# Kernel optimization log

Hardware: AMD Instinct MI355X
Metric: run time of the kernel (lower is better)

## Reference

```python
import jax, jax.numpy as jnp
import numpy as np

D_MODEL = 32
NHEAD = 4
NUM_LAYERS = 4
WINDOW = 256
D_FF = 2 * D_MODEL
INPUT_DIM = 58
MAX_DEPTH = 12
HEAD_OUT = 25


def _layernorm(x, g, b, eps=1e-5):
    m = jnp.mean(x, axis=-1, keepdims=True)
    v = jnp.mean((x - m) ** 2, axis=-1, keepdims=True)
    return (x - m) / jnp.sqrt(v + eps) * g + b


def _layer(h, ipw, ipb, opw, opb, g1, b1, w1, bb1, w2, bb2, g2, b2):
    # Post-norm transformer layer (subclass overrides parent's norm_first path).
    Wn, S, D = h.shape
    dh = D // NHEAD
    qkv = h @ ipw.T + ipb                      # [Wn, S, 3D]
    q, k, v = jnp.split(qkv, 3, axis=-1)
    q = q.reshape(Wn, S, NHEAD, dh).transpose(0, 2, 1, 3)  # [Wn,H,S,dh]
    k = k.reshape(Wn, S, NHEAD, dh).transpose(0, 2, 1, 3)
    v = v.reshape(Wn, S, NHEAD, dh).transpose(0, 2, 1, 3)
    scores = jnp.einsum('whqd,whkd->whqk', q, k) / jnp.sqrt(jnp.asarray(dh, h.dtype))
    a = jax.nn.softmax(scores, axis=-1)        # eager attn weights (need_weights=True path)
    o = jnp.einsum('whqk,whkd->whqd', a, v).transpose(0, 2, 1, 3).reshape(Wn, S, D)
    o = o @ opw.T + opb
    h = _layernorm(h + o, g1, b1)
    ff = jax.nn.gelu(h @ w1.T + bb1, approximate=False) @ w2.T + bb2
    return _layernorm(h + ff, g2, b2)


def setup_inputs() -> dict:
    key = jax.random.key(0)
    ks = jax.random.split(key, 24)
    B, N = 2, 65536
    x = jax.random.uniform(ks[0], (B, N, INPUT_DIM), dtype=jnp.float32)
    layers = jax.random.randint(ks[1], (B, N), 0, MAX_DEPTH)

    def w(k, shape, s=0.05):
        return jax.random.normal(k, shape, jnp.float32) * s

    L = NUM_LAYERS
    return dict(
        x=x,
        layers=layers,
        feature_proj_w=w(ks[2], (D_MODEL, INPUT_DIM)),
        feature_proj_b=w(ks[3], (D_MODEL,)),
        layer_embed=w(ks[4], (MAX_DEPTH, D_MODEL)),
        fourier_B=jax.random.normal(ks[5], (3, D_MODEL // 2), jnp.float32) * 1024.0,
        in_proj_w=w(ks[6], (L, 3 * D_MODEL, D_MODEL)),
        in_proj_b=w(ks[7], (L, 3 * D_MODEL)),
        out_proj_w=w(ks[8], (L, D_MODEL, D_MODEL)),
        out_proj_b=w(ks[9], (L, D_MODEL)),
        ln1_g=jnp.ones((L, D_MODEL), jnp.float32),
        ln1_b=jnp.zeros((L, D_MODEL), jnp.float32),
        lin1_w=w(ks[10], (L, D_FF, D_MODEL)),
        lin1_b=w(ks[11], (L, D_FF)),
        lin2_w=w(ks[12], (L, D_MODEL, D_FF)),
        lin2_b=w(ks[13], (L, D_MODEL)),
        ln2_g=jnp.ones((L, D_MODEL), jnp.float32),
        ln2_b=jnp.zeros((L, D_MODEL), jnp.float32),
        norm_out_g=jnp.ones((D_MODEL,), jnp.float32),
        norm_out_b=jnp.zeros((D_MODEL,), jnp.float32),
        head_w=w(ks[14], (HEAD_OUT, D_MODEL)),
        head_b=w(ks[15], (HEAD_OUT,)),
    )


def reference(x, layers, feature_proj_w, feature_proj_b, layer_embed, fourier_B,
              in_proj_w, in_proj_b, out_proj_w, out_proj_b,
              ln1_g, ln1_b, lin1_w, lin1_b, lin2_w, lin2_b, ln2_g, ln2_b,
              norm_out_g, norm_out_b, head_w, head_b):
    B, N, _ = x.shape
    pos = x[:, :, :3]
    proj = (2.0 * jnp.pi) * (pos @ fourier_B)                  # [B,N,D/2]
    pe = jnp.concatenate([jnp.sin(proj), jnp.cos(proj)], axis=-1)
    h = x @ feature_proj_w.T + feature_proj_b + layer_embed[layers] + pe
    # N chosen divisible by WINDOW, so pad_len == 0 (original pads otherwise)
    nw = N // WINDOW
    h = h.reshape(B * nw, WINDOW, D_MODEL)
    for i in range(NUM_LAYERS):
        h = _layer(h, in_proj_w[i], in_proj_b[i], out_proj_w[i], out_proj_b[i],
                   ln1_g[i], ln1_b[i], lin1_w[i], lin1_b[i], lin2_w[i], lin2_b[i],
                   ln2_g[i], ln2_b[i])
    h = h.reshape(B, N, D_MODEL)
    return _layernorm(h, norm_out_g, norm_out_b) @ head_w.T + head_b
```

## Files before the change

### kernel.cpp

```cpp
#include <hip/hip_runtime.h>

constexpr int S    = 256;
constexpr int D    = 32;
constexpr int NH   = 4;
constexpr int DH   = 8;
constexpr int DFF  = 64;
constexpr int NL   = 4;
constexpr int IND  = 58;
constexpr int HOUT = 25;
constexpr int TPB  = 256;

typedef float  f2 __attribute__((ext_vector_type(2)));
typedef float  f4 __attribute__((ext_vector_type(4)));
typedef __fp16 h2 __attribute__((ext_vector_type(2)));
typedef __fp16 h4 __attribute__((ext_vector_type(4)));

__device__ __forceinline__ f4 MFMA16(h4 a, h4 b, f4 c) {
  return __builtin_amdgcn_mfma_f32_16x16x16f16(a, b, c, 0, 0, 0);
}

constexpr int HOFF  = 0;
constexpr int QKOFF = 16384;
constexpr int VOFF  = 49152;

__device__ __forceinline__ unsigned pk2(float a, float b) {
  h2 h = __builtin_amdgcn_cvt_pkrtz(a, b);
  return __builtin_bit_cast(unsigned, h);
}

__device__ __forceinline__ float exp2fast(float x) {
#if __has_builtin(__builtin_amdgcn_exp2f)
  return __builtin_amdgcn_exp2f(x);
#else
  return exp2f(x);
#endif
}

__device__ __forceinline__ void wave_fence() {
  __builtin_amdgcn_wave_barrier();
  __builtin_amdgcn_sched_barrier(0);
}

template<int NF2>
__device__ __forceinline__ float dotp(const float* __restrict__ w,
                                      const float* __restrict__ v) {
  const f2* W = (const f2*)w;
  const f2* V = (const f2*)v;
  f2 a0 = {0.f, 0.f}, a1 = {0.f, 0.f};
#pragma unroll
  for (int i = 0; i < NF2; i += 2) a0 += V[i] * W[i];
#pragma unroll
  for (int i = 1; i < NF2; i += 2) a1 += V[i] * W[i];
  f2 s = a0 + a1;
  return s.x + s.y;
}

__device__ __forceinline__ float gelu(float x) {
  float u = 2.3022082f * fmaf(0.044715f * x * x, x, x);
  return x * __builtin_amdgcn_rcpf(1.0f + exp2fast(-u));
}

__device__ __forceinline__ void lnorm(float* h, const float* __restrict__ g,
                                      const float* __restrict__ b) {
  f2* hv = (f2*)h;
  f2 s0 = hv[0], s1 = hv[1];
#pragma unroll
  for (int i = 2; i < 16; i += 2) { s0 += hv[i]; s1 += hv[i + 1]; }
  f2 s = s0 + s1;
  const float m = (s.x + s.y) * (1.0f / D);
  const f2 m2 = {m, m};
  f2 v0 = {0.f, 0.f}, v1 = {0.f, 0.f};
#pragma unroll
  for (int i = 0; i < 16; i += 2) {
    f2 c0 = hv[i] - m2;     v0 += c0 * c0;
    f2 c1 = hv[i + 1] - m2; v1 += c1 * c1;
  }
  f2 vs = v0 + v1;
  const float inv = __builtin_amdgcn_rsqf((vs.x + vs.y) * (1.0f / D) + 1e-5f);
  const f2 inv2 = {inv, inv};
  const f2 mi2 = {-m * inv, -m * inv};
  const f2* g2 = (const f2*)g;
  const f2* b2 = (const f2*)b;
#pragma unroll
  for (int i = 0; i < 16; ++i) {
    f2 t = hv[i] * inv2 + mi2;
    hv[i] = t * g2[i] + b2[i];
  }
}

__device__ __forceinline__ void embed_token(
    const float* __restrict__ xrow, int lay,
    const float* __restrict__ fpw, const float* __restrict__ fpb,
    const float* __restrict__ lemb, const float* __restrict__ fB,
    float* __restrict__ h) {
  float xr[IND];
  const f2* xv = (const f2*)xrow;
#pragma unroll
  for (int i = 0; i < 29; ++i) { f2 t = xv[i]; xr[2 * i] = t.x; xr[2 * i + 1] = t.y; }
  const float* le = lemb + lay * D;
  float pe[D];
#pragma unroll
  for (int k = 0; k < 16; ++k) {
    float t = xr[0] * fB[k] + xr[1] * fB[16 + k] + xr[2] * fB[32 + k];
#if __has_builtin(__builtin_amdgcn_sinf) && __has_builtin(__builtin_amdgcn_cosf) && __has_builtin(__builtin_amdgcn_fractf)
    float u = __builtin_amdgcn_fractf(t);
    pe[k]      = __builtin_amdgcn_sinf(u);
    pe[16 + k] = __builtin_amdgcn_cosf(u);
#else
    float sv, cv;
    sincosf(6.2831853071795864f * (t - floorf(t)), &sv, &cv);
    pe[k] = sv; pe[16 + k] = cv;
#endif
  }
#pragma unroll
  for (int d = 0; d < D; ++d)
    h[d] = dotp<29>(fpw + d * IND, xr) + fpb[d] + le[d] + pe[d];
}

__device__ __forceinline__ h4 bfrag(const float* __restrict__ W, int row,
                                    int K, int kh, int quad) {
  f4 w = *(const f4*)(W + row * K + kh * 16 + quad * 4);
  uint2 p{pk2(w.x, w.y), pk2(w.z, w.w)};
  return __builtin_bit_cast(h4, p);
}
__device__ __forceinline__ h4 afrag32(const unsigned char* sm, int base,
                                      int tok, int kh, int quad) {
  return *(const h4*)(sm + base + tok * 64 + (((kh * 4 + quad) ^ (tok & 7)) * 8));
}

__device__ __forceinline__ void store_h16(unsigned char* sm, int tok,
                                          const float* __restrict__ h) {
#pragma unroll
  for (int c = 0; c < 8; ++c) {
    uint2 p{pk2(h[4 * c], h[4 * c + 1]), pk2(h[4 * c + 2], h[4 * c + 3])};
    *(uint2*)(sm + HOFF + tok * 64 + ((c ^ (tok & 7)) * 8)) = p;
  }
}
__device__ __forceinline__ void add_row32(const unsigned char* sm, int base,
                                          int tok, float* __restrict__ h) {
  f2* hv = (f2*)h;
#pragma unroll
  for (int c = 0; c < 8; ++c) {
    h4 q = *(const h4*)(sm + base + tok * 64 + ((c ^ (tok & 7)) * 8));
    f2 lo = {(float)q[0], (float)q[1]};
    f2 hi = {(float)q[2], (float)q[3]};
    hv[2 * c] += lo;
    hv[2 * c + 1] += hi;
  }
}

__global__ void __launch_bounds__(TPB, 2)
spai_fused(const float* __restrict__ x,    const int*   __restrict__ layers,
           const float* __restrict__ fpw,  const float* __restrict__ fpb,
           const float* __restrict__ lemb, const float* __restrict__ fB,
           const float* __restrict__ ipw,  const float* __restrict__ ipb,
           const float* __restrict__ opw,  const float* __restrict__ opb,
           const float* __restrict__ ln1g, const float* __restrict__ ln1b,
           const float* __restrict__ w1,   const float* __restrict__ b1,
           const float* __restrict__ w2,   const float* __restrict__ b2,
           const float* __restrict__ ln2g, const float* __restrict__ ln2b,
           const float* __restrict__ nog,  const float* __restrict__ nob,
           const float* __restrict__ hw,   const float* __restrict__ hb,
           float* __restrict__ out) {
  __shared__ __align__(16) unsigned char sm[65536];
  const int tid  = threadIdx.x;
  const int lane = tid & 63;
  const int wave = tid >> 6;
  const int n16  = lane & 15;
  const int quad = lane >> 4;
  const int qs   = quad & 1;
  const size_t blk_tok = (size_t)blockIdx.x * S;

  float h[D];
  embed_token(x + (blk_tok + tid) * IND, layers[blk_tok + tid],
              fpw, fpb, lemb, fB, h);
  store_h16(sm, tid, h);

  for (int l = 0; l < NL; ++l) {
    __syncthreads();

    const float* Wi = ipw + l * (3 * D) * D;
    const float* Bi = ipb + l * (3 * D);

    {
      h4 Bf[12]; f4 bqk[4]; float bv[2];
#pragma unroll
      for (int nt = 0; nt < 6; ++nt) {
        const float sc = (nt < 2) ? 0.51006973f : 1.0f;
#pragma unroll
        for (int kh = 0; kh < 2; ++kh) {
          f4 wv = *(const f4*)(Wi + (nt * 16 + n16) * D + kh * 16 + quad * 4) * sc;
          uint2 wp{pk2(wv.x, wv.y), pk2(wv.z, wv.w)};
          Bf[nt * 2 + kh] = __builtin_bit_cast(h4, wp);
        }
        if (nt < 4)
          bqk[nt] = *(const f4*)(Bi + nt * 16 + quad * 4) * sc;
        else
          bv[nt - 4] = Bi[nt * 16 + n16];
      }
      h4 Ah[8];
#pragma unroll
      for (int it = 0; it < 4; ++it) {
        const int tok = (wave * 4 + it) * 16 + n16;
        Ah[it * 2]     = afrag32(sm, HOFF, tok, 0, quad);
        Ah[it * 2 + 1] = afrag32(sm, HOFF, tok, 1, quad);
      }
      const int kswz = n16 & 7;
#pragma unroll
      for (int it = 0; it < 4; ++it) {
        const int tok = (wave * 4 + it) * 16 + n16;
#pragma unroll
        for (int nt = 0; nt < 4; ++nt) {
          f4 C = bqk[nt];
          C = MFMA16(Bf[nt * 2], Ah[it * 2], C);
          C = MFMA16(Bf[nt * 2 + 1], Ah[it * 2 + 1], C);
          uint2 p{pk2(C[0], C[1]), pk2(C[2], C[3])};
          *(uint2*)(sm + QKOFF + tok * 128 +
                    (((nt * 2 + (quad >> 1)) ^ kswz) * 16) + (quad & 1) * 8) = p;
        }
#pragma unroll
        for (int nt = 4; nt < 6; ++nt) {
          const float bb = bv[nt - 4];
          f4 C = {bb, bb, bb, bb};
          C = MFMA16(Ah[it * 2], Bf[nt * 2], C);
          C = MFMA16(Ah[it * 2 + 1], Bf[nt * 2 + 1], C);
          uint2 p{pk2(C[0], C[1]), pk2(C[2], C[3])};
          const int vf = (nt - 4) * 16 + n16;
          const int tc = (wave * 4 + it) * 4 + quad;
          *(uint2*)(sm + VOFF + vf * 512 + ((tc ^ ((vf & 7) << 1)) * 8)) = p;
        }
      }
    }
    __syncthreads();

    {
      const int hh  = wave;
      const int m   = n16;
      const int msw = m & 7;
      h4 Kf[16], Vf[16];
      const int kbase = QKOFF + (((4 + hh) ^ msw) * 16) + qs * 8;
#pragma unroll
      for (int jt = 0; jt < 16; ++jt) {
        uint2 a = *(const uint2*)(sm + kbase + (jt * 16 + m) * 128);
        if (quad >= 2) { a.x = 0u; a.y = 0u; }
        Kf[jt] = __builtin_bit_cast(h4, a);
      }
      const unsigned fill = (m == 8) ? 0x3C003C00u : 0u;
      const int vbase = VOFF + (hh * 8 + msw) * 512;
      const int vkey  = msw << 1;
#pragma unroll
      for (int jt = 0; jt < 16; ++jt) {
        uint2 a = *(const uint2*)(sm + vbase + (((jt * 4 + quad) ^ vkey) * 8));
        if (m >= 8) { a.x = fill; a.y = fill; }
        Vf[jt] = __builtin_bit_cast(h4, a);
      }
      const int qoff = QKOFF + ((hh ^ msw) * 16) + qs * 8;
      const int ooff = HOFF + (((hh * 2 + quad) ^ msw) * 8);

#pragma unroll 2
      for (int it = 0; it < 16; ++it) {
        const int ti = it * 16 + m;
        h4 Qf = *(const h4*)(sm + qoff + ti * 128);
        f4 Of0 = {0.f, 0.f, 0.f, 0.f}, Of1 = {0.f, 0.f, 0.f, 0.f};
        const f4 Z = {0.f, 0.f, 0.f, 0.f};
#pragma unroll
        for (int jt = 0; jt < 16; ++jt) {
          f4 T = MFMA16(Kf[jt], Qf, Z);
          uint2 pu{pk2(exp2fast(T[0]), exp2fast(T[1])),
                   pk2(exp2fast(T[2]), exp2fast(T[3]))};
          h4 P = __builtin_bit_cast(h4, pu);
          if (jt & 1) Of1 = MFMA16(Vf[jt], P, Of1);
          else        Of0 = MFMA16(Vf[jt], P, Of0);
        }
        f4 Of = Of0 + Of1;
        float rinv = __builtin_amdgcn_rcpf(Of[0]);
        rinv = __builtin_bit_cast(
            float, __builtin_amdgcn_ds_bpermute(
                       (32 + m) << 2, __builtin_bit_cast(int, rinv)));
        if (quad < 2) {
          f4 o = Of * rinv;
          uint2 p{pk2(o[0], o[1]), pk2(o[2], o[3])};
          *(uint2*)(sm + ooff + ti * 64) = p;
        }
      }
    }
    __syncthreads();

    {
      const float* Wo = opw + l * D * D;
      const float* Bo = opb + l * D;
      h4 Bf[4]; f4 bo[2];
#pragma unroll
      for (int nt = 0; nt < 2; ++nt) {
        bo[nt] = *(const f4*)(Bo + nt * 16 + quad * 4);
#pragma unroll
        for (int kh = 0; kh < 2; ++kh)
          Bf[nt * 2 + kh] = bfrag(Wo, nt * 16 + n16, 32, kh, quad);
      }
      const int kswz = n16 & 7;
#pragma unroll
      for (int ii = 0; ii < 4; ++ii) {
        const int tok = (wave * 4 + ii) * 16 + n16;
        h4 A0 = afrag32(sm, HOFF, tok, 0, quad);
        h4 A1 = afrag32(sm, HOFF, tok, 1, quad);
#pragma unroll
        for (int nt = 0; nt < 2; ++nt) {
          f4 C = bo[nt];
          C = MFMA16(Bf[nt * 2], A0, C);
          C = MFMA16(Bf[nt * 2 + 1], A1, C);
          uint2 p{pk2(C[0], C[1]), pk2(C[2], C[3])};
          *(uint2*)(sm + VOFF + tok * 64 + (((nt * 4 + quad) ^ kswz) * 8)) = p;
        }
      }
    }
    wave_fence();

    add_row32(sm, VOFF, tid, h);
    lnorm(h, ln1g + l * D, ln1b + l * D);
    store_h16(sm, tid, h);
    wave_fence();

    {
      const float* Wa = w1 + l * DFF * D;
      const float* Ba = b1 + l * DFF;
      h4 Bf[8]; f4 ba[4];
#pragma unroll
      for (int ft = 0; ft < 4; ++ft) {
        ba[ft] = *(const f4*)(Ba + ft * 16 + quad * 4);
#pragma unroll
        for (int kh = 0; kh < 2; ++kh)
          Bf[ft * 2 + kh] = bfrag(Wa, ft * 16 + n16, 32, kh, quad);
      }
      const int tswz = n16;
#pragma unroll
      for (int tt = 0; tt < 4; ++tt) {
        const int tok = (wave * 4 + tt) * 16 + n16;
        h4 A0 = afrag32(sm, HOFF, tok, 0, quad);
        h4 A1 = afrag32(sm, HOFF, tok, 1, quad);
#pragma unroll
        for (int ft = 0; ft < 4; ++ft) {
          f4 C = ba[ft];
          C = MFMA16(Bf[ft * 2], A0, C);
          C = MFMA16(Bf[ft * 2 + 1], A1, C);
          uint2 p{pk2(gelu(C[0]), gelu(C[1])), pk2(gelu(C[2]), gelu(C[3]))};
          *(uint2*)(sm + QKOFF + tok * 128 + (((ft * 4 + quad) ^ tswz) * 8)) = p;
        }
      }
    }
    wave_fence();

    {
      const float* Wb = w2 + l * D * DFF;
      const float* Bb = b2 + l * D;
      h4 Bf[8]; f4 bb[2];
#pragma unroll
      for (int nt = 0; nt < 2; ++nt) {
        bb[nt] = *(const f4*)(Bb + nt * 16 + quad * 4);
#pragma unroll
        for (int kh = 0; kh < 4; ++kh)
          Bf[nt * 4 + kh] = bfrag(Wb, nt * 16 + n16, 64, kh, quad);
      }
      const int tswz = n16; const int kswz = n16 & 7;
#pragma unroll
      for (int ii = 0; ii < 4; ++ii) {
        const int tok = (wave * 4 + ii) * 16 + n16;
        h4 A[4];
#pragma unroll
        for (int kh = 0; kh < 4; ++kh)
          A[kh] = *(const h4*)(sm + QKOFF + tok * 128 +
                               (((kh * 4 + quad) ^ tswz) * 8));
#pragma unroll
        for (int nt = 0; nt < 2; ++nt) {
          f4 C = bb[nt];
#pragma unroll
          for (int kh = 0; kh < 4; ++kh) C = MFMA16(Bf[nt * 4 + kh], A[kh], C);
          uint2 p{pk2(C[0], C[1]), pk2(C[2], C[3])};
          *(uint2*)(sm + VOFF + tok * 64 + (((nt * 4 + quad) ^ kswz) * 8)) = p;
        }
      }
    }
    wave_fence();

    add_row32(sm, VOFF, tid, h);
    lnorm(h, ln2g + l * D, ln2b + l * D);
    if (l < NL - 1) store_h16(sm, tid, h);
  }

  __syncthreads();
  lnorm(h, nog, nob);
  float* hs = (float*)sm;
#pragma unroll
  for (int o = 0; o < HOUT; ++o)
    hs[tid * HOUT + o] = dotp<16>(hw + o * D, h) + hb[o];
  __syncthreads();
  f2* og = (f2*)(out + blk_tok * HOUT);
  const f2* os2 = (const f2*)hs;
  for (int i = tid; i < S * HOUT / 2; i += TPB) og[i] = os2[i];
}

extern "C" void kernel_launch(void* const* d_in, const int* in_sizes, int n_in,
                              void* d_out, int out_size, void* d_ws, size_t ws_size,
                              hipStream_t stream) {
  const float* x    = (const float*)d_in[0];
  const int*   lays = (const int*)  d_in[1];
  const float* fpw  = (const float*)d_in[2];
  const float* fpb  = (const float*)d_in[3];
  const float* lemb = (const float*)d_in[4];
  const float* fB   = (const float*)d_in[5];
  const float* ipw  = (const float*)d_in[6];
  const float* ipb  = (const float*)d_in[7];
  const float* opw  = (const float*)d_in[8];
  const float* opb  = (const float*)d_in[9];
  const float* ln1g = (const float*)d_in[10];
  const float* ln1b = (const float*)d_in[11];
  const float* w1   = (const float*)d_in[12];
  const float* b1   = (const float*)d_in[13];
  const float* w2   = (const float*)d_in[14];
  const float* b2   = (const float*)d_in[15];
  const float* ln2g = (const float*)d_in[16];
  const float* ln2b = (const float*)d_in[17];
  const float* nog  = (const float*)d_in[18];
  const float* nob  = (const float*)d_in[19];
  const float* hw   = (const float*)d_in[20];
  const float* hb   = (const float*)d_in[21];
  float* out = (float*)d_out;

  const int nwin = in_sizes[0] / (S * IND);
  spai_fused<<<nwin, TPB, 0, stream>>>(x, lays, fpw, fpb, lemb, fB, ipw, ipb,
                                       opw, opb, ln1g, ln1b, w1, b1, w2, b2,
                                       ln2g, ln2b, nog, nob, hw, hb, out);
}
```

Baseline: 240.5 us.

## Split each token across two threads and fuse FFN GEMMs in registers

Doubles the block to 512 threads so each token's 32-wide hidden state is held by two threads of 16 features each. LayerNorm and the output head combine the two halves with xor-shuffles, and the embedding computes only the half's sine or cosine via a quarter-phase shift. Attention and the projection GEMMs are re-partitioned over 8 waves. Separately, the two FFN matmuls are fused so the GELU outputs stay in registers as MFMA operands instead of round-tripping through shared memory. This trades per-thread register pressure and serial per-token work for more waves per block, at the cost of extra shuffles and duplicated weight-fragment loads per wave.

```diff
diff --git a/kernel.cpp b/kernel.cpp
--- a/kernel.cpp
+++ b/kernel.cpp
@@ -8,7 +8,7 @@
 constexpr int NL   = 4;
 constexpr int IND  = 58;
 constexpr int HOUT = 25;
-constexpr int TPB  = 256;
+constexpr int TPB  = 512;
 
 typedef float  f2 __attribute__((ext_vector_type(2)));
 typedef float  f4 __attribute__((ext_vector_type(4)));
@@ -60,36 +60,40 @@
   return x * __builtin_amdgcn_rcpf(1.0f + exp2fast(-u));
 }
 
-__device__ __forceinline__ void lnorm(float* h, const float* __restrict__ g,
-                                      const float* __restrict__ b) {
+__device__ __forceinline__ void lnorm_half(float* h, const float* __restrict__ g16,
+                                           const float* __restrict__ b16) {
   f2* hv = (f2*)h;
   f2 s0 = hv[0], s1 = hv[1];
 #pragma unroll
-  for (int i = 2; i < 16; i += 2) { s0 += hv[i]; s1 += hv[i + 1]; }
-  f2 s = s0 + s1;
-  const float m = (s.x + s.y) * (1.0f / D);
+  for (int i = 2; i < 8; i += 2) { s0 += hv[i]; s1 += hv[i + 1]; }
+  f2 sv = s0 + s1;
+  float s = sv.x + sv.y;
+  s += __shfl_xor(s, 1);
+  const float m = s * (1.0f / D);
   const f2 m2 = {m, m};
   f2 v0 = {0.f, 0.f}, v1 = {0.f, 0.f};
 #pragma unroll
-  for (int i = 0; i < 16; i += 2) {
+  for (int i = 0; i < 8; i += 2) {
     f2 c0 = hv[i] - m2;     v0 += c0 * c0;
     f2 c1 = hv[i + 1] - m2; v1 += c1 * c1;
   }
-  f2 vs = v0 + v1;
-  const float inv = __builtin_amdgcn_rsqf((vs.x + vs.y) * (1.0f / D) + 1e-5f);
+  f2 vv = v0 + v1;
+  float v = vv.x + vv.y;
+  v += __shfl_xor(v, 1);
+  const float inv = __builtin_amdgcn_rsqf(v * (1.0f / D) + 1e-5f);
   const f2 inv2 = {inv, inv};
   const f2 mi2 = {-m * inv, -m * inv};
-  const f2* g2 = (const f2*)g;
-  const f2* b2 = (const f2*)b;
-#pragma unroll
-  for (int i = 0; i < 16; ++i) {
+  const f2* g2 = (const f2*)g16;
+  const f2* b2 = (const f2*)b16;
+#pragma unroll
+  for (int i = 0; i < 8; ++i) {
     f2 t = hv[i] * inv2 + mi2;
     hv[i] = t * g2[i] + b2[i];
   }
 }
 
-__device__ __forceinline__ void embed_token(
-    const float* __restrict__ xrow, int lay,
+__device__ __forceinline__ void embed_half(
+    const float* __restrict__ xrow, int lay, int half,
     const float* __restrict__ fpw, const float* __restrict__ fpb,
     const float* __restrict__ lemb, const float* __restrict__ fB,
     float* __restrict__ h) {
@@ -97,24 +101,23 @@
   const f2* xv = (const f2*)xrow;
 #pragma unroll
   for (int i = 0; i < 29; ++i) { f2 t = xv[i]; xr[2 * i] = t.x; xr[2 * i + 1] = t.y; }
-  const float* le = lemb + lay * D;
-  float pe[D];
+  const int fo = half * 16;
+  const float* le = lemb + lay * D + fo;
+  const float qsh = 0.25f * half;
+  float pe[16];
 #pragma unroll
   for (int k = 0; k < 16; ++k) {
     float t = xr[0] * fB[k] + xr[1] * fB[16 + k] + xr[2] * fB[32 + k];
-#if __has_builtin(__builtin_amdgcn_sinf) && __has_builtin(__builtin_amdgcn_cosf) && __has_builtin(__builtin_amdgcn_fractf)
-    float u = __builtin_amdgcn_fractf(t);
-    pe[k]      = __builtin_amdgcn_sinf(u);
-    pe[16 + k] = __builtin_amdgcn_cosf(u);
+#if __has_builtin(__builtin_amdgcn_sinf) && __has_builtin(__builtin_amdgcn_fractf)
+    pe[k] = __builtin_amdgcn_sinf(__builtin_amdgcn_fractf(t + qsh));
 #else
-    float sv, cv;
-    sincosf(6.2831853071795864f * (t - floorf(t)), &sv, &cv);
-    pe[k] = sv; pe[16 + k] = cv;
+    float u = t + qsh;
+    pe[k] = sinf(6.2831853071795864f * (u - floorf(u)));
 #endif
   }
 #pragma unroll
-  for (int d = 0; d < D; ++d)
-    h[d] = dotp<29>(fpw + d * IND, xr) + fpb[d] + le[d] + pe[d];
+  for (int dd = 0; dd < 16; ++dd)
+    h[dd] = dotp<29>(fpw + (fo + dd) * IND, xr) + fpb[fo + dd] + le[dd] + pe[dd];
 }
 
 __device__ __forceinline__ h4 bfrag(const float* __restrict__ W, int row,
@@ -128,20 +131,20 @@
   return *(const h4*)(sm + base + tok * 64 + (((kh * 4 + quad) ^ (tok & 7)) * 8));
 }
 
-__device__ __forceinline__ void store_h16(unsigned char* sm, int tok,
-                                          const float* __restrict__ h) {
-#pragma unroll
-  for (int c = 0; c < 8; ++c) {
+__device__ __forceinline__ void store_h16_half(unsigned char* sm, int tok,
+                                               int half, const float* __restrict__ h) {
+#pragma unroll
+  for (int c = 0; c < 4; ++c) {
     uint2 p{pk2(h[4 * c], h[4 * c + 1]), pk2(h[4 * c + 2], h[4 * c + 3])};
-    *(uint2*)(sm + HOFF + tok * 64 + ((c ^ (tok & 7)) * 8)) = p;
-  }
-}
-__device__ __forceinline__ void add_row32(const unsigned char* sm, int base,
-                                          int tok, float* __restrict__ h) {
+    *(uint2*)(sm + HOFF + tok * 64 + (((half * 4 + c) ^ (tok & 7)) * 8)) = p;
+  }
+}
+__device__ __forceinline__ void add_row_half(const unsigned char* sm, int base,
+                                             int tok, int half, float* __restrict__ h) {
   f2* hv = (f2*)h;
 #pragma unroll
-  for (int c = 0; c < 8; ++c) {
-    h4 q = *(const h4*)(sm + base + tok * 64 + ((c ^ (tok & 7)) * 8));
+  for (int c = 0; c < 4; ++c) {
+    h4 q = *(const h4*)(sm + base + tok * 64 + (((half * 4 + c) ^ (tok & 7)) * 8));
     f2 lo = {(float)q[0], (float)q[1]};
     f2 hi = {(float)q[2], (float)q[3]};
     hv[2 * c] += lo;
@@ -149,7 +152,7 @@
   }
 }
 
-__global__ void __launch_bounds__(TPB, 2)
+__global__ void __launch_bounds__(TPB, 4)
 spai_fused(const float* __restrict__ x,    const int*   __restrict__ layers,
            const float* __restrict__ fpw,  const float* __restrict__ fpb,
            const float* __restrict__ lemb, const float* __restrict__ fB,
@@ -163,18 +166,21 @@
            const float* __restrict__ hw,   const float* __restrict__ hb,
            float* __restrict__ out) {
   __shared__ __align__(16) unsigned char sm[65536];
-  const int tid  = threadIdx.x;
-  const int lane = tid & 63;
-  const int wave = tid >> 6;
-  const int n16  = lane & 15;
-  const int quad = lane >> 4;
-  const int qs   = quad & 1;
+  const int tid   = threadIdx.x;
+  const int lane  = tid & 63;
+  const int wave  = tid >> 6;
+  const int n16   = lane & 15;
+  const int quad  = lane >> 4;
+  const int qs    = quad & 1;
+  const int token = tid >> 1;
+  const int half  = tid & 1;
   const size_t blk_tok = (size_t)blockIdx.x * S;
 
-  float h[D];
-  embed_token(x + (blk_tok + tid) * IND, layers[blk_tok + tid],
-              fpw, fpb, lemb, fB, h);
-  store_h16(sm, tid, h);
+  float h[16];
+  embed_half(x + (blk_tok + token) * IND, layers[blk_tok + token], half,
+             fpw, fpb, lemb, fB, h);
+  store_h16_half(sm, token, half, h);
+  wave_fence();
 
   for (int l = 0; l < NL; ++l) {
     __syncthreads();
@@ -198,22 +204,22 @@
         else
           bv[nt - 4] = Bi[nt * 16 + n16];
       }
-      h4 Ah[8];
-#pragma unroll
-      for (int it = 0; it < 4; ++it) {
-        const int tok = (wave * 4 + it) * 16 + n16;
-        Ah[it * 2]     = afrag32(sm, HOFF, tok, 0, quad);
-        Ah[it * 2 + 1] = afrag32(sm, HOFF, tok, 1, quad);
+      h4 Ah[4];
+#pragma unroll
+      for (int ii = 0; ii < 2; ++ii) {
+        const int tok = (wave * 2 + ii) * 16 + n16;
+        Ah[ii * 2]     = afrag32(sm, HOFF, tok, 0, quad);
+        Ah[ii * 2 + 1] = afrag32(sm, HOFF, tok, 1, quad);
       }
       const int kswz = n16 & 7;
 #pragma unroll
-      for (int it = 0; it < 4; ++it) {
-        const int tok = (wave * 4 + it) * 16 + n16;
+      for (int ii = 0; ii < 2; ++ii) {
+        const int tok = (wave * 2 + ii) * 16 + n16;
 #pragma unroll
         for (int nt = 0; nt < 4; ++nt) {
           f4 C = bqk[nt];
-          C = MFMA16(Bf[nt * 2], Ah[it * 2], C);
-          C = MFMA16(Bf[nt * 2 + 1], Ah[it * 2 + 1], C);
+          C = MFMA16(Bf[nt * 2], Ah[ii * 2], C);
+          C = MFMA16(Bf[nt * 2 + 1], Ah[ii * 2 + 1], C);
           uint2 p{pk2(C[0], C[1]), pk2(C[2], C[3])};
           *(uint2*)(sm + QKOFF + tok * 128 +
                     (((nt * 2 + (quad >> 1)) ^ kswz) * 16) + (quad & 1) * 8) = p;
@@ -222,11 +228,11 @@
         for (int nt = 4; nt < 6; ++nt) {
           const float bb = bv[nt - 4];
           f4 C = {bb, bb, bb, bb};
-          C = MFMA16(Ah[it * 2], Bf[nt * 2], C);
-          C = MFMA16(Ah[it * 2 + 1], Bf[nt * 2 + 1], C);
+          C = MFMA16(Ah[ii * 2], Bf[nt * 2], C);
+          C = MFMA16(Ah[ii * 2 + 1], Bf[nt * 2 + 1], C);
           uint2 p{pk2(C[0], C[1]), pk2(C[2], C[3])};
           const int vf = (nt - 4) * 16 + n16;
-          const int tc = (wave * 4 + it) * 4 + quad;
+          const int tc = (wave * 2 + ii) * 4 + quad;
           *(uint2*)(sm + VOFF + vf * 512 + ((tc ^ ((vf & 7) << 1)) * 8)) = p;
         }
       }
@@ -234,7 +240,8 @@
     __syncthreads();
 
     {
-      const int hh  = wave;
+      const int hh  = wave >> 1;
+      const int sub = wave & 1;
       const int m   = n16;
       const int msw = m & 7;
       h4 Kf[16], Vf[16];
@@ -258,7 +265,8 @@
       const int ooff = HOFF + (((hh * 2 + quad) ^ msw) * 8);
 
 #pragma unroll 2
-      for (int it = 0; it < 16; ++it) {
+      for (int i2 = 0; i2 < 8; ++i2) {
+        const int it = sub * 8 + i2;
         const int ti = it * 16 + m;
         h4 Qf = *(const h4*)(sm + qoff + ti * 128);
         f4 Of0 = {0.f, 0.f, 0.f, 0.f}, Of1 = {0.f, 0.f, 0.f, 0.f};
@@ -299,8 +307,8 @@
       }
       const int kswz = n16 & 7;
 #pragma unroll
-      for (int ii = 0; ii < 4; ++ii) {
-        const int tok = (wave * 4 + ii) * 16 + n16;
+      for (int ii = 0; ii < 2; ++ii) {
+        const int tok = (wave * 2 + ii) * 16 + n16;
         h4 A0 = afrag32(sm, HOFF, tok, 0, quad);
         h4 A1 = afrag32(sm, HOFF, tok, 1, quad);
 #pragma unroll
@@ -315,83 +323,73 @@
     }
     wave_fence();
 
-    add_row32(sm, VOFF, tid, h);
-    lnorm(h, ln1g + l * D, ln1b + l * D);
-    store_h16(sm, tid, h);
+    add_row_half(sm, VOFF, token, half, h);
+    lnorm_half(h, ln1g + l * D + half * 16, ln1b + l * D + half * 16);
+    store_h16_half(sm, token, half, h);
     wave_fence();
 
     {
       const float* Wa = w1 + l * DFF * D;
       const float* Ba = b1 + l * DFF;
-      h4 Bf[8]; f4 ba[4];
+      const float* Wb = w2 + l * D * DFF;
+      const float* Bb = b2 + l * D;
+      h4 WaF[8]; f4 ba[4]; h4 WbF[8]; f4 bb[2];
 #pragma unroll
       for (int ft = 0; ft < 4; ++ft) {
         ba[ft] = *(const f4*)(Ba + ft * 16 + quad * 4);
 #pragma unroll
         for (int kh = 0; kh < 2; ++kh)
-          Bf[ft * 2 + kh] = bfrag(Wa, ft * 16 + n16, 32, kh, quad);
-      }
-      const int tswz = n16;
-#pragma unroll
-      for (int tt = 0; tt < 4; ++tt) {
-        const int tok = (wave * 4 + tt) * 16 + n16;
+          WaF[ft * 2 + kh] = bfrag(Wa, ft * 16 + n16, 32, kh, quad);
+      }
+#pragma unroll
+      for (int nt = 0; nt < 2; ++nt) {
+        bb[nt] = *(const f4*)(Bb + nt * 16 + quad * 4);
+#pragma unroll
+        for (int kh = 0; kh < 4; ++kh)
+          WbF[nt * 4 + kh] = bfrag(Wb, nt * 16 + n16, 64, kh, quad);
+      }
+      const int kswz = n16 & 7;
+#pragma unroll
+      for (int tt = 0; tt < 2; ++tt) {
+        const int tok = (wave * 2 + tt) * 16 + n16;
         h4 A0 = afrag32(sm, HOFF, tok, 0, quad);
         h4 A1 = afrag32(sm, HOFF, tok, 1, quad);
+        h4 Pf[4];
 #pragma unroll
         for (int ft = 0; ft < 4; ++ft) {
           f4 C = ba[ft];
-          C = MFMA16(Bf[ft * 2], A0, C);
-          C = MFMA16(Bf[ft * 2 + 1], A1, C);
+          C = MFMA16(WaF[ft * 2], A0, C);
+          C = MFMA16(WaF[ft * 2 + 1], A1, C);
           uint2 p{pk2(gelu(C[0]), gelu(C[1])), pk2(gelu(C[2]), gelu(C[3]))};
-          *(uint2*)(sm + QKOFF + tok * 128 + (((ft * 4 + quad) ^ tswz) * 8)) = p;
+          Pf[ft] = __builtin_bit_cast(h4, p);
+        }
+#pragma unroll
+        for (int nt = 0; nt < 2; ++nt) {
+          f4 C = bb[nt];
+#pragma unroll
+          for (int ft = 0; ft < 4; ++ft) C = MFMA16(WbF[nt * 4 + ft], Pf[ft], C);
+          uint2 p{pk2(C[0], C[1]), pk2(C[2], C[3])};
+          *(uint2*)(sm + VOFF + tok * 64 + (((nt * 4 + quad) ^ kswz) * 8)) = p;
         }
       }
     }
     wave_fence();
 
-    {
-      const float* Wb = w2 + l * D * DFF;
-      const float* Bb = b2 + l * D;
-      h4 Bf[8]; f4 bb[2];
-#pragma unroll
-      for (int nt = 0; nt < 2; ++nt) {
-        bb[nt] = *(const f4*)(Bb + nt * 16 + quad * 4);
-#pragma unroll
-        for (int kh = 0; kh < 4; ++kh)
-          Bf[nt * 4 + kh] = bfrag(Wb, nt * 16 + n16, 64, kh, quad);
-      }
-      const int tswz = n16; const int kswz = n16 & 7;
-#pragma unroll
-      for (int ii = 0; ii < 4; ++ii) {
-        const int tok = (wave * 4 + ii) * 16 + n16;
-        h4 A[4];
-#pragma unroll
-        for (int kh = 0; kh < 4; ++kh)
-          A[kh] = *(const h4*)(sm + QKOFF + tok * 128 +
-                               (((kh * 4 + quad) ^ tswz) * 8));
-#pragma unroll
-        for (int nt = 0; nt < 2; ++nt) {
-          f4 C = bb[nt];
-#pragma unroll
-          for (int kh = 0; kh < 4; ++kh) C = MFMA16(Bf[nt * 4 + kh], A[kh], C);
-          uint2 p{pk2(C[0], C[1]), pk2(C[2], C[3])};
-          *(uint2*)(sm + VOFF + tok * 64 + (((nt * 4 + quad) ^ kswz) * 8)) = p;
-        }
-      }
-    }
+    add_row_half(sm, VOFF, token, half, h);
+    lnorm_half(h, ln2g + l * D + half * 16, ln2b + l * D + half * 16);
+    if (l < NL - 1) store_h16_half(sm, token, half, h);
     wave_fence();
-
-    add_row32(sm, VOFF, tid, h);
-    lnorm(h, ln2g + l * D, ln2b + l * D);
-    if (l < NL - 1) store_h16(sm, tid, h);
   }
 
   __syncthreads();
-  lnorm(h, nog, nob);
+  lnorm_half(h, nog + half * 16, nob + half * 16);
   float* hs = (float*)sm;
 #pragma unroll
-  for (int o = 0; o < HOUT; ++o)
-    hs[tid * HOUT + o] = dotp<16>(hw + o * D, h) + hb[o];
+  for (int o = 0; o < HOUT; ++o) {
+    float p = dotp<8>(hw + o * D + half * 16, h);
+    p += __shfl_xor(p, 1);
+    if ((o < 13) == (half == 0)) hs[token * HOUT + o] = p + hb[o];
+  }
   __syncthreads();
   f2* og = (f2*)(out + blk_tok * HOUT);
   const f2* os2 = (const f2*)hs;
```

Result: slower. 338.8 us (+40.9%).

## Fuse FFN GEMMs in registers and prefetch layer weights before attention

Applied to the files above, without the earlier changes.

The FFN first-layer output (after GELU) now feeds the second FFN GEMM directly from registers, because the MFMA accumulator layout matches the B-operand fragment layout. This removes the LDS round-trip through QKOFF and one wave fence. All out-proj and FFN weight fragments and biases are now loaded at the start of each layer, before the QKV/attention phase, so their global-load latency overlaps with attention work. The cost is higher register pressure across the attention section, which may reduce occupancy or cause spills.

```diff
diff --git a/kernel.cpp b/kernel.cpp
--- a/kernel.cpp
+++ b/kernel.cpp
@@ -182,6 +182,39 @@
     const float* Wi = ipw + l * (3 * D) * D;
     const float* Bi = ipb + l * (3 * D);
 
+    h4 WoF[4]; f4 bo2[2];
+    h4 WaF[8]; f4 ba4[4];
+    h4 WbF[8]; f4 bb2[2];
+    {
+      const float* Wo = opw + l * D * D;
+      const float* Bo = opb + l * D;
+#pragma unroll
+      for (int nt = 0; nt < 2; ++nt) {
+        bo2[nt] = *(const f4*)(Bo + nt * 16 + quad * 4);
+#pragma unroll
+        for (int kh = 0; kh < 2; ++kh)
+          WoF[nt * 2 + kh] = bfrag(Wo, nt * 16 + n16, 32, kh, quad);
+      }
+      const float* Wa = w1 + l * DFF * D;
+      const float* Ba = b1 + l * DFF;
+#pragma unroll
+      for (int ft = 0; ft < 4; ++ft) {
+        ba4[ft] = *(const f4*)(Ba + ft * 16 + quad * 4);
+#pragma unroll
+        for (int kh = 0; kh < 2; ++kh)
+          WaF[ft * 2 + kh] = bfrag(Wa, ft * 16 + n16, 32, kh, quad);
+      }
+      const float* Wb = w2 + l * D * DFF;
+      const float* Bb = b2 + l * D;
+#pragma unroll
+      for (int nt = 0; nt < 2; ++nt) {
+        bb2[nt] = *(const f4*)(Bb + nt * 16 + quad * 4);
+#pragma unroll
+        for (int kh = 0; kh < 4; ++kh)
+          WbF[nt * 4 + kh] = bfrag(Wb, nt * 16 + n16, 64, kh, quad);
+      }
+    }
+
     {
       h4 Bf[12]; f4 bqk[4]; float bv[2];
 #pragma unroll
@@ -287,16 +320,6 @@
     __syncthreads();
 
     {
-      const float* Wo = opw + l * D * D;
-      const float* Bo = opb + l * D;
-      h4 Bf[4]; f4 bo[2];
-#pragma unroll
-      for (int nt = 0; nt < 2; ++nt) {
-        bo[nt] = *(const f4*)(Bo + nt * 16 + quad * 4);
-#pragma unroll
-        for (int kh = 0; kh < 2; ++kh)
-          Bf[nt * 2 + kh] = bfrag(Wo, nt * 16 + n16, 32, kh, quad);
-      }
       const int kswz = n16 & 7;
 #pragma unroll
       for (int ii = 0; ii < 4; ++ii) {
@@ -305,9 +328,9 @@
         h4 A1 = afrag32(sm, HOFF, tok, 1, quad);
 #pragma unroll
         for (int nt = 0; nt < 2; ++nt) {
-          f4 C = bo[nt];
-          C = MFMA16(Bf[nt * 2], A0, C);
-          C = MFMA16(Bf[nt * 2 + 1], A1, C);
+          f4 C = bo2[nt];
+          C = MFMA16(WoF[nt * 2], A0, C);
+          C = MFMA16(WoF[nt * 2 + 1], A1, C);
           uint2 p{pk2(C[0], C[1]), pk2(C[2], C[3])};
           *(uint2*)(sm + VOFF + tok * 64 + (((nt * 4 + quad) ^ kswz) * 8)) = p;
         }
@@ -321,59 +344,26 @@
     wave_fence();
 
     {
-      const float* Wa = w1 + l * DFF * D;
-      const float* Ba = b1 + l * DFF;
-      h4 Bf[8]; f4 ba[4];
-#pragma unroll
-      for (int ft = 0; ft < 4; ++ft) {
-        ba[ft] = *(const f4*)(Ba + ft * 16 + quad * 4);
-#pragma unroll
-        for (int kh = 0; kh < 2; ++kh)
-          Bf[ft * 2 + kh] = bfrag(Wa, ft * 16 + n16, 32, kh, quad);
-      }
-      const int tswz = n16;
+      const int kswz = n16 & 7;
 #pragma unroll
       for (int tt = 0; tt < 4; ++tt) {
         const int tok = (wave * 4 + tt) * 16 + n16;
         h4 A0 = afrag32(sm, HOFF, tok, 0, quad);
         h4 A1 = afrag32(sm, HOFF, tok, 1, quad);
+        h4 Pf[4];
 #pragma unroll
         for (int ft = 0; ft < 4; ++ft) {
-          f4 C = ba[ft];
-          C = MFMA16(Bf[ft * 2], A0, C);
-          C = MFMA16(Bf[ft * 2 + 1], A1, C);
+          f4 C = ba4[ft];
+          C = MFMA16(WaF[ft * 2], A0, C);
+          C = MFMA16(WaF[ft * 2 + 1], A1, C);
           uint2 p{pk2(gelu(C[0]), gelu(C[1])), pk2(gelu(C[2]), gelu(C[3]))};
-          *(uint2*)(sm + QKOFF + tok * 128 + (((ft * 4 + quad) ^ tswz) * 8)) = p;
-        }
-      }
-    }
-    wave_fence();
-
-    {
-      const float* Wb = w2 + l * D * DFF;
-      const float* Bb = b2 + l * D;
-      h4 Bf[8]; f4 bb[2];
-#pragma unroll
-      for (int nt = 0; nt < 2; ++nt) {
-        bb[nt] = *(const f4*)(Bb + nt * 16 + quad * 4);
-#pragma unroll
-        for (int kh = 0; kh < 4; ++kh)
-          Bf[nt * 4 + kh] = bfrag(Wb, nt * 16 + n16, 64, kh, quad);
-      }
-      const int tswz = n16; const int kswz = n16 & 7;
-#pragma unroll
-      for (int ii = 0; ii < 4; ++ii) {
-        const int tok = (wave * 4 + ii) * 16 + n16;
-        h4 A[4];
-#pragma unroll
-        for (int kh = 0; kh < 4; ++kh)
-          A[kh] = *(const h4*)(sm + QKOFF + tok * 128 +
-                               (((kh * 4 + quad) ^ tswz) * 8));
+          Pf[ft] = __builtin_bit_cast(h4, p);
+        }
 #pragma unroll
         for (int nt = 0; nt < 2; ++nt) {
-          f4 C = bb[nt];
-#pragma unroll
-          for (int kh = 0; kh < 4; ++kh) C = MFMA16(Bf[nt * 4 + kh], A[kh], C);
+          f4 C = bb2[nt];
+#pragma unroll
+          for (int ft = 0; ft < 4; ++ft) C = MFMA16(WbF[nt * 4 + ft], Pf[ft], C);
           uint2 p{pk2(C[0], C[1]), pk2(C[2], C[3])};
           *(uint2*)(sm + VOFF + tok * 64 + (((nt * 4 + quad) ^ kswz) * 8)) = p;
         }
```

Result: no change. 245.1 us (+1.9%).
